# Performance work log

Measured on AMD Instinct MI355X. Metric: run time of the kernel, lower is better.

Reference implementation:

```python
import jax, jax.numpy as jnp
import numpy as np

N_NODES = 100000
N_GRAPHS = 64
EPS = 1e-5


def _sage_conv(x, src, dst, Wl, bl, Wr):
    # mean-aggregate neighbor messages (src -> dst), then lin_l(agg) + lin_r(x)
    n = x.shape[0]
    deg = jax.ops.segment_sum(jnp.ones_like(dst, dtype=x.dtype), dst, num_segments=n)
    agg = jax.ops.segment_sum(x[src], dst, num_segments=n)  # [N, d]
    agg = agg / jnp.maximum(deg, 1.0)[:, None]
    return agg @ Wl + bl + x @ Wr


def _bn_relu(x, gamma, beta):
    mu = jnp.mean(x, axis=0)
    var = jnp.var(x, axis=0)
    return jax.nn.relu((x - mu) * jax.lax.rsqrt(var + EPS) * gamma + beta)


def setup_inputs() -> dict:
    key = jax.random.key(0)
    ks = jax.random.split(key, 16)
    E = 1600000
    x = jax.random.normal(ks[0], (N_NODES, 2), dtype=jnp.float32)
    edge_index = jax.random.randint(ks[1], (2, E), 0, N_NODES, dtype=jnp.int64)
    batch = jnp.sort(jax.random.randint(ks[2], (N_NODES,), 0, N_GRAPHS, dtype=jnp.int64))

    def lin(k, din, dout):
        s = 1.0 / np.sqrt(din)
        return jax.random.uniform(k, (din, dout), jnp.float32, -s, s)

    d = {"x": x, "edge_index": edge_index, "batch": batch}
    dims = [(2, 32), (32, 64), (64, 128)]
    for i, (din, dout) in enumerate(dims, 1):
        k1, k2 = jax.random.split(ks[2 + i])
        d[f"Wl{i}"] = lin(k1, din, dout)
        d[f"bl{i}"] = jnp.zeros((dout,), jnp.float32)
        d[f"Wr{i}"] = lin(k2, din, dout)
        d[f"g{i}"] = jnp.ones((dout,), jnp.float32)
        d[f"be{i}"] = jnp.zeros((dout,), jnp.float32)
    d["Wf1"] = lin(ks[10], 128, 64)
    d["bf1"] = jnp.zeros((64,), jnp.float32)
    d["Wf2"] = lin(ks[11], 64, 1)
    d["bf2"] = jnp.zeros((1,), jnp.float32)
    return d


def reference(x, edge_index, batch,
              Wl1, bl1, Wr1, g1, be1,
              Wl2, bl2, Wr2, g2, be2,
              Wl3, bl3, Wr3, g3, be3,
              Wf1, bf1, Wf2, bf2):
    src, dst = edge_index[0], edge_index[1]
    h = _bn_relu(_sage_conv(x, src, dst, Wl1, bl1, Wr1), g1, be1)
    h = _bn_relu(_sage_conv(h, src, dst, Wl2, bl2, Wr2), g2, be2)
    h = _bn_relu(_sage_conv(h, src, dst, Wl3, bl3, Wr3), g3, be3)
    # global mean pool over graphs
    cnt = jax.ops.segment_sum(jnp.ones_like(batch, dtype=h.dtype), batch, num_segments=N_GRAPHS)
    pooled = jax.ops.segment_sum(h, batch, num_segments=N_GRAPHS) / jnp.maximum(cnt, 1.0)[:, None]
    out = jax.nn.relu(pooled @ Wf1 + bf1)
    # dropout is identity in eval mode
    return out @ Wf2 + bf2
```

## Files before the change

### kernel.cpp

```cpp
#include <hip/hip_runtime.h>
#include <hip/hip_fp16.h>

#define N_NODES 100000
#define N_GRAPHS 64
#define BN_EPS 1e-5

#define NB 782
#define NC 49
#define PT1 4096
#define PT2 2048
#define BPC 16
#define CAP 3072

typedef _Float16 f16x8 __attribute__((ext_vector_type(8)));
typedef float f32x4 __attribute__((ext_vector_type(4)));

union F16x8u {
    f16x8 v;
    __half2 h2[4];
    uint4 u;
};

__device__ __forceinline__ float bfly64(float v) {
#pragma unroll
    for (int m = 1; m < 64; m <<= 1) v += __shfl_xor(v, m, 64);
    return v;
}

__device__ __forceinline__ unsigned pack_h2(float a, float b) {
    __half2 h = __floats2half2_rn(a, b);
    unsigned w;
    __builtin_memcpy(&w, &h, 4);
    return w;
}

__device__ __forceinline__ float2 unpack_h2(unsigned w) {
    __half2 h;
    __builtin_memcpy(&h, &w, 4);
    return __half22float2(h);
}

__global__ void hist_fine(const int* __restrict__ dst, int* __restrict__ bhist, int E) {
    __shared__ int h[NB];
    for (int i = threadIdx.x; i < NB; i += 256) h[i] = 0;
    __syncthreads();
    int stride = gridDim.x * 256;
    for (int e = blockIdx.x * 256 + threadIdx.x; e < E; e += stride) {
        int d = __builtin_nontemporal_load(dst + e);
        atomicAdd(&h[d >> 7], 1);
    }
    __syncthreads();
    for (int i = threadIdx.x; i < NB; i += 256)
        if (h[i]) atomicAdd(&bhist[i], h[i]);
}

__global__ void scan_buckets(const int* __restrict__ bhist, int* __restrict__ bo,
                             int* __restrict__ fcur, int* __restrict__ co,
                             int* __restrict__ ccur) {
    __shared__ int sh[1024];
    int t = threadIdx.x;
    sh[t] = (t < NB) ? bhist[t] : 0;
    __syncthreads();
    for (int st = 1; st < 1024; st <<= 1) {
        int v = (t >= st) ? sh[t - st] : 0;
        __syncthreads();
        sh[t] += v;
        __syncthreads();
    }
    int total = sh[NB - 1];
    if (t < NB) {
        int e = t ? sh[t - 1] : 0;
        bo[t] = e; fcur[t] = e;
    } else if (t < 784) {
        if (t == NB) bo[NB] = total;
        fcur[t] = total;
    }
    if (t < NC) {
        int i = t << 4;
        int e = i ? sh[i - 1] : 0;
        co[t] = e; ccur[t] = e;
    } else if (t == NC) {
        co[NC] = total;
    }
}

__global__ __launch_bounds__(256)
void part1(const int* __restrict__ dst, const int* __restrict__ src,
           int* __restrict__ ccur, int* __restrict__ cdst, int* __restrict__ csrc, int E) {
    __shared__ int ld[PT1], ls[PT1];
    __shared__ unsigned char lb[PT1];
    __shared__ int hist[NC], lbase[NC], gbase[NC];
    long long t0 = (long long)blockIdx.x * PT1;
    int n = (int)min((long long)PT1, (long long)E - t0);
    int tid = threadIdx.x;
    for (int i = tid; i < NC; i += 256) hist[i] = 0;
    __syncthreads();
    int d[PT1 / 256], s[PT1 / 256], c[PT1 / 256];
#pragma unroll
    for (int k = 0; k < PT1 / 256; ++k) {
        int li = k * 256 + tid;
        if (li < n) {
            d[k] = __builtin_nontemporal_load(dst + t0 + li);
            s[k] = __builtin_nontemporal_load(src + t0 + li);
            c[k] = d[k] >> 11;
            atomicAdd(&hist[c[k]], 1);
        }
    }
    __syncthreads();
    if (tid == 0) {
        int run = 0;
        for (int i = 0; i < NC; ++i) { lbase[i] = run; run += hist[i]; }
    }
    __syncthreads();
    if (tid < NC) gbase[tid] = atomicAdd(&ccur[tid], hist[tid]);
    __syncthreads();
    for (int i = tid; i < NC; i += 256) hist[i] = 0;
    __syncthreads();
#pragma unroll
    for (int k = 0; k < PT1 / 256; ++k) {
        int li = k * 256 + tid;
        if (li < n) {
            int pos = lbase[c[k]] + atomicAdd(&hist[c[k]], 1);
            ld[pos] = d[k]; ls[pos] = s[k]; lb[pos] = (unsigned char)c[k];
        }
    }
    __syncthreads();
    for (int i = tid; i < n; i += 256) {
        int bb = lb[i];
        int g = gbase[bb] + (i - lbase[bb]);
        cdst[g] = ld[i];
        csrc[g] = ls[i];
    }
}

__global__ __launch_bounds__(256)
void part2(const int* __restrict__ cdst, const int* __restrict__ csrc,
           const int* __restrict__ co, int* __restrict__ fcur,
           int* __restrict__ qdst, int* __restrict__ qsrc) {
    __shared__ int ld[PT2], ls[PT2];
    __shared__ unsigned char lb[PT2];
    __shared__ int hist[16], lbase[16], gbase[16];
    int c = blockIdx.x / BPC;
    int j = blockIdx.x % BPC;
    int beg = co[c], end = co[c + 1];
    int tid = threadIdx.x;
    for (int t0 = beg + j * PT2; t0 < end; t0 += BPC * PT2) {
        int n = min(PT2, end - t0);
        if (tid < 16) hist[tid] = 0;
        __syncthreads();
        int d[PT2 / 256], s[PT2 / 256], f[PT2 / 256];
#pragma unroll
        for (int k = 0; k < PT2 / 256; ++k) {
            int li = k * 256 + tid;
            if (li < n) {
                d[k] = cdst[t0 + li];
                s[k] = csrc[t0 + li];
                f[k] = (d[k] >> 7) & 15;
                atomicAdd(&hist[f[k]], 1);
            }
        }
        __syncthreads();
        if (tid == 0) {
            int run = 0;
            for (int i = 0; i < 16; ++i) { lbase[i] = run; run += hist[i]; }
        }
        __syncthreads();
        if (tid < 16) gbase[tid] = atomicAdd(&fcur[(c << 4) + tid], hist[tid]);
        __syncthreads();
        if (tid < 16) hist[tid] = 0;
        __syncthreads();
#pragma unroll
        for (int k = 0; k < PT2 / 256; ++k) {
            int li = k * 256 + tid;
            if (li < n) {
                int pos = lbase[f[k]] + atomicAdd(&hist[f[k]], 1);
                ld[pos] = d[k]; ls[pos] = s[k]; lb[pos] = (unsigned char)f[k];
            }
        }
        __syncthreads();
        for (int i = tid; i < n; i += 256) {
            int bb = lb[i];
            int g = gbase[bb] + (i - lbase[bb]);
            qdst[g] = ld[i];
            qsrc[g] = ls[i];
        }
        __syncthreads();
    }
}

__global__ __launch_bounds__(256)
void fill_final(const int* __restrict__ qdst, const int* __restrict__ qsrc,
                const int* __restrict__ bo, int* __restrict__ offs,
                int* __restrict__ nbr, int N, int E) {
    __shared__ int cnt[128], cbase[128], cur[128];
    __shared__ int lout[CAP];
    int b = blockIdx.x;
    int nlo = b << 7;
    int nn = min(128, N - nlo);
    int ebeg = bo[b], ne = bo[b + 1] - ebeg;
    int tid = threadIdx.x;
    if (tid < 128) { cnt[tid] = 0; cur[tid] = 0; }
    __syncthreads();
    for (int i = tid; i < ne; i += 256)
        atomicAdd(&cnt[qdst[ebeg + i] - nlo], 1);
    __syncthreads();
    if (tid < 128) cbase[tid] = cnt[tid];
    __syncthreads();
    for (int st = 1; st < 128; st <<= 1) {
        int v = 0;
        if (tid < 128 && tid >= st) v = cbase[tid - st];
        __syncthreads();
        if (tid < 128 && tid >= st) cbase[tid] += v;
        __syncthreads();
    }
    if (tid < nn)
        offs[nlo + tid] = ebeg + (tid ? cbase[tid - 1] : 0);
    if (b == NB - 1 && tid == 0) offs[N] = E;
    __syncthreads();
    for (int i = tid; i < ne; i += 256) {
        int d = qdst[ebeg + i];
        int s = qsrc[ebeg + i];
        int ln = d - nlo;
        int p = (ln ? cbase[ln - 1] : 0) + atomicAdd(&cur[ln], 1);
        lout[p] = s;
    }
    __syncthreads();
    for (int i = tid; i < ne; i += 256)
        nbr[ebeg + i] = lout[i];
}

__global__ __launch_bounds__(256)
void layer1_fused(const float2* __restrict__ x2,
                  const int* __restrict__ offs, const int* __restrict__ nbr,
                  const float* __restrict__ Wl, const float* __restrict__ bl,
                  const float* __restrict__ Wr,
                  __half* __restrict__ hout16,
                  double* __restrict__ sums, int N) {
    __shared__ float sAr[64];
    int tid = threadIdx.x;
    if (tid < 64) sAr[tid] = 0.f;
    __syncthreads();
    int n = blockIdx.x * 256 + tid;
    bool valid = (n < N);
    int beg = 0, end = 0;
    if (valid) { beg = offs[n]; end = offs[n + 1]; }
    double ax = 0.0, ay = 0.0;
    int j = beg;
    for (; j + 4 <= end; j += 4) {
        int s0 = nbr[j], s1 = nbr[j + 1], s2 = nbr[j + 2], s3 = nbr[j + 3];
        float2 v0 = x2[s0], v1 = x2[s1], v2 = x2[s2], v3 = x2[s3];
        ax += v0.x; ay += v0.y;
        ax += v1.x; ay += v1.y;
        ax += v2.x; ay += v2.y;
        ax += v3.x; ay += v3.y;
    }
    for (; j < end; ++j) {
        float2 v = x2[nbr[j]];
        ax += v.x; ay += v.y;
    }
    float invd = 1.0f / fmaxf((float)(end - beg), 1.0f);
    float a0 = (float)ax * invd, a1 = (float)ay * invd;
    float x0 = 0.f, x1 = 0.f;
    if (valid) {
        float2 xv = x2[n];
        x0 = xv.x; x1 = xv.y;
    }
    float acc[32];
#pragma unroll
    for (int jj = 0; jj < 32; ++jj)
        acc[jj] = bl[jj] + a0 * Wl[jj] + a1 * Wl[32 + jj] + x0 * Wr[jj] + x1 * Wr[32 + jj];
    if (valid) {
        unsigned w[16];
#pragma unroll
        for (int p = 0; p < 16; ++p) w[p] = pack_h2(acc[2*p], acc[2*p+1]);
        uint4* q = (uint4*)(hout16 + (size_t)n * 32);
        q[0] = make_uint4(w[0], w[1], w[2], w[3]);
        q[1] = make_uint4(w[4], w[5], w[6], w[7]);
        q[2] = make_uint4(w[8], w[9], w[10], w[11]);
        q[3] = make_uint4(w[12], w[13], w[14], w[15]);
    }
    int lane = tid & 63;
#pragma unroll
    for (int jj = 0; jj < 32; ++jj) {
        float v = valid ? acc[jj] : 0.f;
        float s = bfly64(v);
        float q = bfly64(v * v);
        if (lane == jj) atomicAdd(&sAr[jj], s);
        if (lane == 32 + jj) atomicAdd(&sAr[32 + jj], q);
    }
    __syncthreads();
    if (tid < 64) atomicAdd(&sums[tid], (double)sAr[tid]);
}

template<int F>
__global__ __launch_bounds__(256)
void bn_apply(const uint4* __restrict__ h, const double* __restrict__ sums,
              const float* __restrict__ gamma, const float* __restrict__ beta,
              uint4* __restrict__ out, int N) {
    __shared__ __align__(16) float lsc[F], lsf[F];
    int tid = threadIdx.x;
    if (tid < F) {
        double mu = sums[tid] / (double)N_NODES;
        double var = sums[F + tid] / (double)N_NODES - mu * mu;
        if (var < 0.0) var = 0.0;
        double sc = (double)gamma[tid] / sqrt(var + BN_EPS);
        lsc[tid] = (float)sc;
        lsf[tid] = (float)((double)beta[tid] - mu * sc);
    }
    __syncthreads();
    constexpr int FV = F / 8;
    int total = N * FV;
    for (int i = blockIdx.x * 256 + tid; i < total; i += gridDim.x * 256) {
        uint4 v = h[i];
        int c4 = (i & (FV - 1)) * 2;
        float4 sca = ((const float4*)lsc)[c4];
        float4 scb = ((const float4*)lsc)[c4 + 1];
        float4 sfa = ((const float4*)lsf)[c4];
        float4 sfb = ((const float4*)lsf)[c4 + 1];
        float2 f0 = unpack_h2(v.x), f1 = unpack_h2(v.y);
        float2 f2 = unpack_h2(v.z), f3 = unpack_h2(v.w);
        uint4 o;
        o.x = pack_h2(fmaxf(f0.x * sca.x + sfa.x, 0.f), fmaxf(f0.y * sca.y + sfa.y, 0.f));
        o.y = pack_h2(fmaxf(f1.x * sca.z + sfa.z, 0.f), fmaxf(f1.y * sca.w + sfa.w, 0.f));
        o.z = pack_h2(fmaxf(f2.x * scb.x + sfb.x, 0.f), fmaxf(f2.y * scb.y + sfb.y, 0.f));
        o.w = pack_h2(fmaxf(f3.x * scb.z + sfb.z, 0.f), fmaxf(f3.y * scb.w + sfb.w, 0.f));
        out[i] = o;
    }
}

template<int F>
__global__ __launch_bounds__(256)
void agg_sum(const uint4* __restrict__ xb, const int* __restrict__ offs,
             const int* __restrict__ nbr, uint4* __restrict__ aggh, int N) {
    constexpr int FV = F / 8;
    constexpr int NPB = 256 / FV;
    int n = blockIdx.x * NPB + threadIdx.y;
    if (n >= N) return;
    int f = threadIdx.x;
    int beg = offs[n], end = offs[n + 1];
    float a0[8], a1[8];
#pragma unroll
    for (int q = 0; q < 8; ++q) { a0[q] = 0.f; a1[q] = 0.f; }
    int j = beg;
    for (; j + 8 <= end; j += 8) {
        int s[8];
#pragma unroll
        for (int u = 0; u < 8; ++u) s[u] = __builtin_nontemporal_load(nbr + j + u);
        uint4 v[8];
#pragma unroll
        for (int u = 0; u < 8; ++u) v[u] = xb[s[u] * FV + f];
#pragma unroll
        for (int u = 0; u < 8; ++u) {
            float* acc = (u & 1) ? a1 : a0;
            float2 f0 = unpack_h2(v[u].x), f1 = unpack_h2(v[u].y);
            float2 f2 = unpack_h2(v[u].z), f3 = unpack_h2(v[u].w);
            acc[0] += f0.x; acc[1] += f0.y; acc[2] += f1.x; acc[3] += f1.y;
            acc[4] += f2.x; acc[5] += f2.y; acc[6] += f3.x; acc[7] += f3.y;
        }
    }
    for (; j < end; ++j) {
        int s = __builtin_nontemporal_load(nbr + j);
        uint4 v = xb[s * FV + f];
        float2 f0 = unpack_h2(v.x), f1 = unpack_h2(v.y);
        float2 f2 = unpack_h2(v.z), f3 = unpack_h2(v.w);
        a0[0] += f0.x; a0[1] += f0.y; a0[2] += f1.x; a0[3] += f1.y;
        a0[4] += f2.x; a0[5] += f2.y; a0[6] += f3.x; a0[7] += f3.y;
    }
    float invd = 1.0f / fmaxf((float)(end - beg), 1.0f);
    uint4 o;
    o.x = pack_h2((a0[0] + a1[0]) * invd, (a0[1] + a1[1]) * invd);
    o.y = pack_h2((a0[2] + a1[2]) * invd, (a0[3] + a1[3]) * invd);
    o.z = pack_h2((a0[4] + a1[4]) * invd, (a0[5] + a1[5]) * invd);
    o.w = pack_h2((a0[6] + a1[6]) * invd, (a0[7] + a1[7]) * invd);
    aggh[n * FV + f] = o;
}

__global__ __launch_bounds__(256)
void pack_w(const float* __restrict__ Wl2, const float* __restrict__ Wr2,
            const float* __restrict__ Wl3, const float* __restrict__ Wr3,
            __half* __restrict__ pk) {
    int e = blockIdx.x * 256 + threadIdx.x;
    const float* W; int le, DOUT, NCB, base, SZ;
    if (e < 2048)       { W = Wl2; le = e;         DOUT = 64;  NCB = 4; base = 0;     SZ = 2048; }
    else if (e < 4096)  { W = Wr2; le = e - 2048;  DOUT = 64;  NCB = 4; base = 4096;  SZ = 2048; }
    else if (e < 12288) { W = Wl3; le = e - 4096;  DOUT = 128; NCB = 8; base = 8192;  SZ = 8192; }
    else                { W = Wr3; le = e - 12288; DOUT = 128; NCB = 8; base = 24576; SZ = 8192; }
    int i = le & 7;
    int lane = (le >> 3) & 63;
    int cbkb = le >> 9;
    int cb = cbkb % NCB;
    int kb = cbkb / NCB;
    int k = kb * 32 + ((lane >> 4) << 3) + i;
    int col = cb * 16 + (lane & 15);
    float w = W[k * DOUT + col];
    __half h = __float2half(w);
    float lo = w - __half2float(h);
    pk[base + le] = h;
    pk[base + SZ + le] = __float2half(lo);
}

template<int DIN, int DOUT>
__global__ __launch_bounds__(256)
void linear_mfma(const __half* __restrict__ bnx16, const __half* __restrict__ agg16,
                 const __half* __restrict__ wlhi, const __half* __restrict__ wllo,
                 const __half* __restrict__ wrhi, const __half* __restrict__ wrlo,
                 const float* __restrict__ bl,
                 __half* __restrict__ hout16, float* __restrict__ partial, int N) {
    constexpr int KB = DIN / 32;
    constexpr int NCB = DOUT / 16;
    constexpr int MREP = 2;
    constexpr int MB = 4 * MREP * 16;
    __shared__ float blkS[DOUT], blkQ[DOUT];
    int tid = threadIdx.x;
    for (int i = tid; i < DOUT; i += 256) { blkS[i] = 0.f; blkQ[i] = 0.f; }
    __syncthreads();
    int n0 = blockIdx.x * MB;

    int wave = tid >> 6;
    int lane = tid & 63;
    int rlane = lane & 15;
    int kg = lane >> 4;
    int rbase = n0 + wave * (MREP * 16);

    f16x8 aA[MREP][KB], aX[MREP][KB];
#pragma unroll
    for (int m = 0; m < MREP; ++m) {
        int row = rbase + m * 16 + rlane;
        int rowc = min(row, N - 1);
#pragma unroll
        for (int kb = 0; kb < KB; ++kb) {
            int c0 = kb * 32 + kg * 8;
            F16x8u ta, tx;
            ta.u = *(const uint4*)(agg16 + (size_t)rowc * DIN + c0);
            tx.u = *(const uint4*)(bnx16 + (size_t)rowc * DIN + c0);
            aA[m][kb] = ta.v;
            aX[m][kb] = tx.v;
        }
    }

    f32x4 acc[MREP][NCB];
#pragma unroll
    for (int cb = 0; cb < NCB; ++cb) {
        float bv = bl[cb * 16 + rlane];
#pragma unroll
        for (int m = 0; m < MREP; ++m)
            acc[m][cb] = {bv, bv, bv, bv};
    }

#pragma unroll
    for (int cb = 0; cb < NCB; ++cb) {
#pragma unroll
        for (int kb = 0; kb < KB; ++kb) {
            size_t fo = ((size_t)(kb * NCB + cb) * 64 + lane) * 8;
            f16x8 blh = *(const f16x8*)(wlhi + fo);
            f16x8 bll = *(const f16x8*)(wllo + fo);
            f16x8 brh = *(const f16x8*)(wrhi + fo);
            f16x8 brl = *(const f16x8*)(wrlo + fo);
#pragma unroll
            for (int m = 0; m < MREP; ++m) {
                acc[m][cb] = __builtin_amdgcn_mfma_f32_16x16x32_f16(aA[m][kb], blh, acc[m][cb], 0, 0, 0);
                acc[m][cb] = __builtin_amdgcn_mfma_f32_16x16x32_f16(aA[m][kb], bll, acc[m][cb], 0, 0, 0);
                acc[m][cb] = __builtin_amdgcn_mfma_f32_16x16x32_f16(aX[m][kb], brh, acc[m][cb], 0, 0, 0);
                acc[m][cb] = __builtin_amdgcn_mfma_f32_16x16x32_f16(aX[m][kb], brl, acc[m][cb], 0, 0, 0);
            }
        }
    }

#pragma unroll
    for (int m = 0; m < MREP; ++m) {
        int rowb = rbase + m * 16 + kg * 4;
#pragma unroll
        for (int r = 0; r < 4; ++r) {
            int node = rowb + r;
            if (node < N) {
#pragma unroll
                for (int cb = 0; cb < NCB; ++cb)
                    hout16[(size_t)node * DOUT + cb * 16 + rlane] = __float2half(acc[m][cb][r]);
            }
        }
    }

#pragma unroll
    for (int cb = 0; cb < NCB; ++cb) {
        float s = 0.f, q = 0.f;
#pragma unroll
        for (int m = 0; m < MREP; ++m) {
            int rowb = rbase + m * 16 + kg * 4;
#pragma unroll
            for (int r = 0; r < 4; ++r) {
                if (rowb + r < N) {
                    float v = acc[m][cb][r];
                    s += v; q += v * v;
                }
            }
        }
        s += __shfl_xor(s, 16, 64); s += __shfl_xor(s, 32, 64);
        q += __shfl_xor(q, 16, 64); q += __shfl_xor(q, 32, 64);
        if (kg == 0) {
            atomicAdd(&blkS[cb * 16 + rlane], s);
            atomicAdd(&blkQ[cb * 16 + rlane], q);
        }
    }
    __syncthreads();
    float* po = partial + (size_t)blockIdx.x * (2 * DOUT);
    for (int i = tid; i < DOUT; i += 256) {
        po[i] = blkS[i];
        po[DOUT + i] = blkQ[i];
    }
}

template<int F>
__global__ __launch_bounds__(256)
void stats_finalize2(const float* __restrict__ partial, double* __restrict__ sums, int P) {
    __shared__ double sh[256];
    int i = blockIdx.x;
    int t = threadIdx.x;
    double a = 0.0;
    for (int k = t; k < P; k += 256)
        a += (double)partial[(size_t)k * (2 * F) + i];
    sh[t] = a;
    __syncthreads();
    for (int st = 128; st > 0; st >>= 1) {
        if (t < st) sh[t] += sh[t + st];
        __syncthreads();
    }
    if (t == 0) sums[i] = sh[0];
}

__global__ void pool_partial(const __half* __restrict__ h, const int* __restrict__ batch,
                             const double* __restrict__ sums,
                             const float* __restrict__ gamma, const float* __restrict__ beta,
                             double* __restrict__ pooled_d, int N) {
    __shared__ float lsc[128], lsf[128];
    const int CH = 64;
    int f = threadIdx.x;
    {
        double mu = sums[f] / (double)N_NODES;
        double var = sums[128 + f] / (double)N_NODES - mu * mu;
        if (var < 0.0) var = 0.0;
        double sc = (double)gamma[f] / sqrt(var + BN_EPS);
        lsc[f] = (float)sc;
        lsf[f] = (float)((double)beta[f] - mu * sc);
    }
    __syncthreads();
    int n0 = blockIdx.x * CH;
    if (n0 >= N) return;
    int n1 = min(n0 + CH, N);
    float sc = lsc[f], sf = lsf[f];
    int g = batch[n0];
    float acc = 0.f;
    for (int n = n0; n < n1; ++n) {
        int bg = batch[n];
        if (bg != g) {
            atomicAdd(&pooled_d[g * 128 + f], (double)acc);
            acc = 0.f;
            g = bg;
        }
        float v = __half2float(h[(long long)n * 128 + f]);
        acc += fmaxf(v * sc + sf, 0.f);
    }
    atomicAdd(&pooled_d[g * 128 + f], (double)acc);
}

__global__ void mlp_fused(const double* __restrict__ pooled_d, const int* __restrict__ batch,
                          const float* __restrict__ Wf1, const float* __restrict__ bf1,
                          const float* __restrict__ Wf2, const float* __restrict__ bf2,
                          float* __restrict__ out, int N) {
    __shared__ float sp[128];
    int g = blockIdx.x;
    int t = threadIdx.x;
    int lo = 0, hi = N;
    while (lo < hi) { int m = (lo + hi) >> 1; if (batch[m] < g) lo = m + 1; else hi = m; }
    int start = lo;
    hi = N;
    while (lo < hi) { int m = (lo + hi) >> 1; if (batch[m] < g + 1) lo = m + 1; else hi = m; }
    int cnt = lo - start;
    sp[t] = (float)(pooled_d[g * 128 + t] / (double)max(cnt, 1));
    __syncthreads();
    if (t < 64) {
        float hacc = bf1[t];
#pragma unroll 8
        for (int k = 0; k < 128; ++k) hacc += sp[k] * Wf1[k * 64 + t];
        hacc = fmaxf(hacc, 0.f) * Wf2[t];
        for (int o = 32; o > 0; o >>= 1) hacc += __shfl_down(hacc, o);
        if (t == 0) out[g] = hacc + bf2[0];
    }
}

extern "C" void kernel_launch(void* const* d_in, const int* in_sizes, int n_in,
                              void* d_out, int out_size, void* d_ws, size_t ws_size,
                              hipStream_t stream) {
    const float* x     = (const float*)d_in[0];
    const int*   ei    = (const int*)d_in[1];
    const int*   batch = (const int*)d_in[2];
    const float *Wl1=(const float*)d_in[3],  *bl1=(const float*)d_in[4],  *Wr1=(const float*)d_in[5];
    const float *g1 =(const float*)d_in[6],  *be1=(const float*)d_in[7];
    const float *Wl2=(const float*)d_in[8],  *bl2=(const float*)d_in[9],  *Wr2=(const float*)d_in[10];
    const float *g2 =(const float*)d_in[11], *be2=(const float*)d_in[12];
    const float *Wl3=(const float*)d_in[13], *bl3=(const float*)d_in[14], *Wr3=(const float*)d_in[15];
    const float *g3 =(const float*)d_in[16], *be3=(const float*)d_in[17];
    const float *Wf1=(const float*)d_in[18], *bf1=(const float*)d_in[19];
    const float *Wf2=(const float*)d_in[20], *bf2=(const float*)d_in[21];

    const int N = N_NODES;
    const int E = in_sizes[1] / 2;
    const int* src = ei;
    const int* dst = ei + E;

    char* ws = (char*)d_ws;
    size_t off = 0;
    auto salloc = [&](size_t bytes) {
        void* p = ws + off;
        off += (bytes + 255) & ~(size_t)255;
        return p;
    };
    int*    bhist   = (int*)   salloc(NB * 4);
    double* sums    = (double*)salloc(768 * 8);
    double* pooledd = (double*)salloc((size_t)N_GRAPHS * 128 * 8);
    size_t zero_bytes = off;
    int*    offs    = (int*)   salloc((size_t)(N + 1) * 4);
    int*    bo      = (int*)   salloc((NB + 1) * 4);
    int*    fcur    = (int*)   salloc(784 * 4);
    int*    co      = (int*)   salloc((NC + 1) * 4);
    int*    ccur    = (int*)   salloc(NC * 4);
    int*    nbr     = (int*)   salloc((size_t)E * 4);
    float*  partial = (float*) salloc((size_t)1024 * 256 * 4);
    __half* pk      = (__half*)salloc((size_t)40960 * 2);
    __half* h1h     = (__half*)salloc((size_t)(N + 256) * 32 * 2);
    __half* b1h     = (__half*)salloc((size_t)(N + 256) * 32 * 2);
    __half* h2h     = (__half*)salloc((size_t)(N + 256) * 64 * 2);
    __half* b2h     = (__half*)salloc((size_t)(N + 256) * 64 * 2);
    __half* h3h     = (__half*)salloc((size_t)(N + 256) * 128 * 2);
    __half* aggh    = (__half*)salloc((size_t)(N + 256) * 64 * 2);
    (void)ws_size;

    double* sums1 = sums, *sums2 = sums + 256, *sums3 = sums + 512;
    int* cdst = (int*)h3h;
    int* csrc = cdst + E;
    int* qdst = (int*)aggh;
    int* qsrc = qdst + E;

    const __half *pwl2h = pk,         *pwl2l = pk + 2048;
    const __half *pwr2h = pk + 4096,  *pwr2l = pk + 6144;
    const __half *pwl3h = pk + 8192,  *pwl3l = pk + 16384;
    const __half *pwr3h = pk + 24576, *pwr3l = pk + 32768;

    hipMemsetAsync(bhist, 0, zero_bytes, stream);

    pack_w<<<80, 256, 0, stream>>>(Wl2, Wr2, Wl3, Wr3, pk);

    hist_fine<<<1024, 256, 0, stream>>>(dst, bhist, E);
    scan_buckets<<<1, 1024, 0, stream>>>(bhist, bo, fcur, co, ccur);
    part1<<<(E + PT1 - 1) / PT1, 256, 0, stream>>>(dst, src, ccur, cdst, csrc, E);
    part2<<<NC * BPC, 256, 0, stream>>>(cdst, csrc, co, fcur, qdst, qsrc);
    fill_final<<<NB, 256, 0, stream>>>(qdst, qsrc, bo, offs, nbr, N, E);

    const int NL = (N + 255) / 256;
    const int NBLK = (N + 127) / 128;

    layer1_fused<<<NL, 256, 0, stream>>>((const float2*)x, offs, nbr,
                                          Wl1, bl1, Wr1, h1h, sums1, N);

    bn_apply<32><<<512, 256, 0, stream>>>((const uint4*)h1h, sums1, g1, be1, (uint4*)b1h, N);
    agg_sum<32><<<(N + 63) / 64, dim3(4, 64), 0, stream>>>(
        (const uint4*)b1h, offs, nbr, (uint4*)aggh, N);
    linear_mfma<32, 64><<<NBLK, 256, 0, stream>>>(
        b1h, (const __half*)aggh, pwl2h, pwl2l, pwr2h, pwr2l, bl2, h2h, partial, N);
    stats_finalize2<64><<<128, 256, 0, stream>>>(partial, sums2, NBLK);

    bn_apply<64><<<512, 256, 0, stream>>>((const uint4*)h2h, sums2, g2, be2, (uint4*)b2h, N);
    agg_sum<64><<<(N + 31) / 32, dim3(8, 32), 0, stream>>>(
        (const uint4*)b2h, offs, nbr, (uint4*)aggh, N);
    linear_mfma<64, 128><<<NBLK, 256, 0, stream>>>(
        b2h, (const __half*)aggh, pwl3h, pwl3l, pwr3h, pwr3l, bl3, h3h, partial, N);
    stats_finalize2<128><<<256, 256, 0, stream>>>(partial, sums3, NBLK);

    pool_partial<<<(N + 63) / 64, 128, 0, stream>>>(h3h, batch, sums3, g3, be3, pooledd, N);
    mlp_fused<<<N_GRAPHS, 128, 0, stream>>>(pooledd, batch, Wf1, bf1, Wf2, bf2, (float*)d_out, N);
}
```

Before: 347.6 us.

## Gather neighbor features in FP8 with mean quantization-error correction

The BN-apply kernels now also write an FP8 copy of each activated feature row. They accumulate the per-feature quantization error and add it to a global buffer. The aggregation kernels gather these FP8 rows instead of FP16, which halves the bytes per random neighbor read, then add the mean error back as a bias correction. This trades gather bandwidth for extra FP8 writes, an atomic error reduction, and lower per-edge precision that the global mean correction only partly compensates.

```diff
diff --git a/kernel.cpp b/kernel.cpp
--- a/kernel.cpp
+++ b/kernel.cpp
@@ -14,6 +14,7 @@
 
 typedef _Float16 f16x8 __attribute__((ext_vector_type(8)));
 typedef float f32x4 __attribute__((ext_vector_type(4)));
+typedef float f32x2 __attribute__((ext_vector_type(2)));
 
 union F16x8u {
     f16x8 v;
@@ -296,8 +297,11 @@
 __global__ __launch_bounds__(256)
 void bn_apply(const uint4* __restrict__ h, const double* __restrict__ sums,
               const float* __restrict__ gamma, const float* __restrict__ beta,
-              uint4* __restrict__ out, int N) {
+              uint4* __restrict__ out, uint2* __restrict__ out8,
+              float* __restrict__ qerr, int N) {
+    constexpr int FV = F / 8;
     __shared__ __align__(16) float lsc[F], lsf[F];
+    __shared__ float eacc[4 * F];
     int tid = threadIdx.x;
     if (tid < F) {
         double mu = sums[tid] / (double)N_NODES;
@@ -308,7 +312,9 @@
         lsf[tid] = (float)((double)beta[tid] - mu * sc);
     }
     __syncthreads();
-    constexpr int FV = F / 8;
+    float eloc[8];
+#pragma unroll
+    for (int j = 0; j < 8; ++j) eloc[j] = 0.f;
     int total = N * FV;
     for (int i = blockIdx.x * 256 + tid; i < total; i += gridDim.x * 256) {
         uint4 v = h[i];
@@ -319,28 +325,70 @@
         float4 sfb = ((const float4*)lsf)[c4 + 1];
         float2 f0 = unpack_h2(v.x), f1 = unpack_h2(v.y);
         float2 f2 = unpack_h2(v.z), f3 = unpack_h2(v.w);
+        float r0 = fmaxf(f0.x * sca.x + sfa.x, 0.f), r1 = fmaxf(f0.y * sca.y + sfa.y, 0.f);
+        float r2 = fmaxf(f1.x * sca.z + sfa.z, 0.f), r3 = fmaxf(f1.y * sca.w + sfa.w, 0.f);
+        float r4 = fmaxf(f2.x * scb.x + sfb.x, 0.f), r5 = fmaxf(f2.y * scb.y + sfb.y, 0.f);
+        float r6 = fmaxf(f3.x * scb.z + sfb.z, 0.f), r7 = fmaxf(f3.y * scb.w + sfb.w, 0.f);
         uint4 o;
-        o.x = pack_h2(fmaxf(f0.x * sca.x + sfa.x, 0.f), fmaxf(f0.y * sca.y + sfa.y, 0.f));
-        o.y = pack_h2(fmaxf(f1.x * sca.z + sfa.z, 0.f), fmaxf(f1.y * sca.w + sfa.w, 0.f));
-        o.z = pack_h2(fmaxf(f2.x * scb.x + sfb.x, 0.f), fmaxf(f2.y * scb.y + sfb.y, 0.f));
-        o.w = pack_h2(fmaxf(f3.x * scb.z + sfb.z, 0.f), fmaxf(f3.y * scb.w + sfb.w, 0.f));
+        o.x = pack_h2(r0, r1);
+        o.y = pack_h2(r2, r3);
+        o.z = pack_h2(r4, r5);
+        o.w = pack_h2(r6, r7);
         out[i] = o;
-    }
+        unsigned q0 = __builtin_amdgcn_cvt_pk_fp8_f32(r0, r1, 0u, false);
+        q0 = __builtin_amdgcn_cvt_pk_fp8_f32(r2, r3, q0, true);
+        unsigned q1 = __builtin_amdgcn_cvt_pk_fp8_f32(r4, r5, 0u, false);
+        q1 = __builtin_amdgcn_cvt_pk_fp8_f32(r6, r7, q1, true);
+        out8[i] = make_uint2(q0, q1);
+        f32x2 d;
+        d = __builtin_amdgcn_cvt_pk_f32_fp8(q0, false); eloc[0] += r0 - d.x; eloc[1] += r1 - d.y;
+        d = __builtin_amdgcn_cvt_pk_f32_fp8(q0, true);  eloc[2] += r2 - d.x; eloc[3] += r3 - d.y;
+        d = __builtin_amdgcn_cvt_pk_f32_fp8(q1, false); eloc[4] += r4 - d.x; eloc[5] += r5 - d.y;
+        d = __builtin_amdgcn_cvt_pk_f32_fp8(q1, true);  eloc[6] += r6 - d.x; eloc[7] += r7 - d.y;
+    }
+    for (int m = FV; m < 64; m <<= 1) {
+#pragma unroll
+        for (int j = 0; j < 8; ++j) eloc[j] += __shfl_xor(eloc[j], m, 64);
+    }
+    int wave = tid >> 6;
+    int lane = tid & 63;
+    if (lane < FV) {
+#pragma unroll
+        for (int j = 0; j < 8; ++j) eacc[wave * F + lane * 8 + j] = eloc[j];
+    }
+    __syncthreads();
+    if (tid < F) {
+        float s = eacc[tid] + eacc[F + tid] + eacc[2 * F + tid] + eacc[3 * F + tid];
+        atomicAdd(&qerr[tid], s);
+    }
+}
+
+__device__ __forceinline__ void accum16_fp8(float* acc, uint4 v) {
+    f32x2 p;
+    p = __builtin_amdgcn_cvt_pk_f32_fp8(v.x, false); acc[0] += p.x;  acc[1] += p.y;
+    p = __builtin_amdgcn_cvt_pk_f32_fp8(v.x, true);  acc[2] += p.x;  acc[3] += p.y;
+    p = __builtin_amdgcn_cvt_pk_f32_fp8(v.y, false); acc[4] += p.x;  acc[5] += p.y;
+    p = __builtin_amdgcn_cvt_pk_f32_fp8(v.y, true);  acc[6] += p.x;  acc[7] += p.y;
+    p = __builtin_amdgcn_cvt_pk_f32_fp8(v.z, false); acc[8] += p.x;  acc[9] += p.y;
+    p = __builtin_amdgcn_cvt_pk_f32_fp8(v.z, true);  acc[10] += p.x; acc[11] += p.y;
+    p = __builtin_amdgcn_cvt_pk_f32_fp8(v.w, false); acc[12] += p.x; acc[13] += p.y;
+    p = __builtin_amdgcn_cvt_pk_f32_fp8(v.w, true);  acc[14] += p.x; acc[15] += p.y;
 }
 
 template<int F>
 __global__ __launch_bounds__(256)
-void agg_sum(const uint4* __restrict__ xb, const int* __restrict__ offs,
-             const int* __restrict__ nbr, uint4* __restrict__ aggh, int N) {
-    constexpr int FV = F / 8;
-    constexpr int NPB = 256 / FV;
+void agg_q(const uint4* __restrict__ xq, const int* __restrict__ offs,
+           const int* __restrict__ nbr, const float* __restrict__ qerr,
+           __half* __restrict__ aggh, int N) {
+    constexpr int FV8 = F / 16;
+    constexpr int NPB = 256 / FV8;
     int n = blockIdx.x * NPB + threadIdx.y;
     if (n >= N) return;
     int f = threadIdx.x;
     int beg = offs[n], end = offs[n + 1];
-    float a0[8], a1[8];
-#pragma unroll
-    for (int q = 0; q < 8; ++q) { a0[q] = 0.f; a1[q] = 0.f; }
+    float a0[16], a1[16];
+#pragma unroll
+    for (int q = 0; q < 16; ++q) { a0[q] = 0.f; a1[q] = 0.f; }
     int j = beg;
     for (; j + 8 <= end; j += 8) {
         int s[8];
@@ -348,31 +396,33 @@
         for (int u = 0; u < 8; ++u) s[u] = __builtin_nontemporal_load(nbr + j + u);
         uint4 v[8];
 #pragma unroll
-        for (int u = 0; u < 8; ++u) v[u] = xb[s[u] * FV + f];
-#pragma unroll
-        for (int u = 0; u < 8; ++u) {
-            float* acc = (u & 1) ? a1 : a0;
-            float2 f0 = unpack_h2(v[u].x), f1 = unpack_h2(v[u].y);
-            float2 f2 = unpack_h2(v[u].z), f3 = unpack_h2(v[u].w);
-            acc[0] += f0.x; acc[1] += f0.y; acc[2] += f1.x; acc[3] += f1.y;
-            acc[4] += f2.x; acc[5] += f2.y; acc[6] += f3.x; acc[7] += f3.y;
-        }
+        for (int u = 0; u < 8; ++u) v[u] = xq[s[u] * FV8 + f];
+#pragma unroll
+        for (int u = 0; u < 8; ++u)
+            accum16_fp8((u & 1) ? a1 : a0, v[u]);
     }
     for (; j < end; ++j) {
         int s = __builtin_nontemporal_load(nbr + j);
-        uint4 v = xb[s * FV + f];
-        float2 f0 = unpack_h2(v.x), f1 = unpack_h2(v.y);
-        float2 f2 = unpack_h2(v.z), f3 = unpack_h2(v.w);
-        a0[0] += f0.x; a0[1] += f0.y; a0[2] += f1.x; a0[3] += f1.y;
-        a0[4] += f2.x; a0[5] += f2.y; a0[6] += f3.x; a0[7] += f3.y;
+        uint4 v = xq[s * FV8 + f];
+        accum16_fp8(a0, v);
     }
     float invd = 1.0f / fmaxf((float)(end - beg), 1.0f);
-    uint4 o;
-    o.x = pack_h2((a0[0] + a1[0]) * invd, (a0[1] + a1[1]) * invd);
-    o.y = pack_h2((a0[2] + a1[2]) * invd, (a0[3] + a1[3]) * invd);
-    o.z = pack_h2((a0[4] + a1[4]) * invd, (a0[5] + a1[5]) * invd);
-    o.w = pack_h2((a0[6] + a1[6]) * invd, (a0[7] + a1[7]) * invd);
-    aggh[n * FV + f] = o;
+    const float invN = (float)(1.0 / (double)N_NODES);
+    float dl[16];
+#pragma unroll
+    for (int k = 0; k < 4; ++k) {
+        float4 d4 = ((const float4*)qerr)[f * 4 + k];
+        dl[4*k] = d4.x * invN; dl[4*k+1] = d4.y * invN;
+        dl[4*k+2] = d4.z * invN; dl[4*k+3] = d4.w * invN;
+    }
+    unsigned w[8];
+#pragma unroll
+    for (int q = 0; q < 8; ++q)
+        w[q] = pack_h2((a0[2*q] + a1[2*q]) * invd + dl[2*q],
+                       (a0[2*q+1] + a1[2*q+1]) * invd + dl[2*q+1]);
+    uint4* op = (uint4*)(aggh + (size_t)n * F + f * 16);
+    op[0] = make_uint4(w[0], w[1], w[2], w[3]);
+    op[1] = make_uint4(w[4], w[5], w[6], w[7]);
 }
 
 __global__ __launch_bounds__(256)
@@ -617,6 +667,7 @@
     int*    bhist   = (int*)   salloc(NB * 4);
     double* sums    = (double*)salloc(768 * 8);
     double* pooledd = (double*)salloc((size_t)N_GRAPHS * 128 * 8);
+    float*  qerr    = (float*) salloc(256 * 4);
     size_t zero_bytes = off;
     int*    offs    = (int*)   salloc((size_t)(N + 1) * 4);
     int*    bo      = (int*)   salloc((NB + 1) * 4);
@@ -628,13 +679,17 @@
     __half* pk      = (__half*)salloc((size_t)40960 * 2);
     __half* h1h     = (__half*)salloc((size_t)(N + 256) * 32 * 2);
     __half* b1h     = (__half*)salloc((size_t)(N + 256) * 32 * 2);
+    unsigned char* b1q = (unsigned char*)salloc((size_t)(N + 256) * 32);
     __half* h2h     = (__half*)salloc((size_t)(N + 256) * 64 * 2);
     __half* b2h     = (__half*)salloc((size_t)(N + 256) * 64 * 2);
+    unsigned char* b2q = (unsigned char*)salloc((size_t)(N + 256) * 64);
     __half* h3h     = (__half*)salloc((size_t)(N + 256) * 128 * 2);
     __half* aggh    = (__half*)salloc((size_t)(N + 256) * 64 * 2);
     (void)ws_size;
 
     double* sums1 = sums, *sums2 = sums + 256, *sums3 = sums + 512;
+    float* qerr1 = qerr;
+    float* qerr2 = qerr + 128;
     int* cdst = (int*)h3h;
     int* csrc = cdst + E;
     int* qdst = (int*)aggh;
@@ -661,16 +716,18 @@
     layer1_fused<<<NL, 256, 0, stream>>>((const float2*)x, offs, nbr,
                                           Wl1, bl1, Wr1, h1h, sums1, N);
 
-    bn_apply<32><<<512, 256, 0, stream>>>((const uint4*)h1h, sums1, g1, be1, (uint4*)b1h, N);
-    agg_sum<32><<<(N + 63) / 64, dim3(4, 64), 0, stream>>>(
-        (const uint4*)b1h, offs, nbr, (uint4*)aggh, N);
+    bn_apply<32><<<512, 256, 0, stream>>>((const uint4*)h1h, sums1, g1, be1,
+                                          (uint4*)b1h, (uint2*)b1q, qerr1, N);
+    agg_q<32><<<(N + 127) / 128, dim3(2, 128), 0, stream>>>(
+        (const uint4*)b1q, offs, nbr, qerr1, (__half*)aggh, N);
     linear_mfma<32, 64><<<NBLK, 256, 0, stream>>>(
         b1h, (const __half*)aggh, pwl2h, pwl2l, pwr2h, pwr2l, bl2, h2h, partial, N);
     stats_finalize2<64><<<128, 256, 0, stream>>>(partial, sums2, NBLK);
 
-    bn_apply<64><<<512, 256, 0, stream>>>((const uint4*)h2h, sums2, g2, be2, (uint4*)b2h, N);
-    agg_sum<64><<<(N + 31) / 32, dim3(8, 32), 0, stream>>>(
-        (const uint4*)b2h, offs, nbr, (uint4*)aggh, N);
+    bn_apply<64><<<512, 256, 0, stream>>>((const uint4*)h2h, sums2, g2, be2,
+                                          (uint4*)b2h, (uint2*)b2q, qerr2, N);
+    agg_q<64><<<(N + 63) / 64, dim3(4, 64), 0, stream>>>(
+        (const uint4*)b2q, offs, nbr, qerr2, (__half*)aggh, N);
     linear_mfma<64, 128><<<NBLK, 256, 0, stream>>>(
         b2h, (const __half*)aggh, pwl3h, pwl3l, pwr3h, pwr3l, bl3, h3h, partial, N);
     stats_finalize2<128><<<256, 256, 0, stream>>>(partial, sums3, NBLK);
```

Measured after the change: 352.8 us. Within noise of the previous version (+1.5%).
